# Kernel optimization log

Measured on AMD Instinct MI355X. Metric: run time of the kernel, lower is better.

Reference implementation:

```python
import jax, jax.numpy as jnp
import numpy as np

BIG = 1e10
RADIUS = 0.5
NSAMPLE = 1


def square_distance(src, dst):
    # src: [B,N,3], dst: [B,M,3] -> [B,N,M] squared euclidean distances
    d = -2.0 * jnp.einsum('bnc,bmc->bnm', src, dst)
    d = d + jnp.sum(src ** 2, -1)[:, :, None]
    d = d + jnp.sum(dst ** 2, -1)[:, None, :]
    return d


def farthest_point_sample(xyz, npoint):
    # xyz: [B,N,3]; returns int32 indices [B,npoint]
    B, N, _ = xyz.shape
    dist0 = jnp.full((B, N), BIG, dtype=xyz.dtype)
    far0 = jnp.argmax(xyz[:, :, 0], axis=1).astype(jnp.int32)

    def step(carry, _):
        dist, far = carry
        centroid = jnp.take_along_axis(xyz, far[:, None, None], axis=1)  # [B,1,3]
        d = jnp.sum((xyz - centroid) ** 2, -1)  # [B,N]
        dist = jnp.minimum(dist, d)
        new_far = jnp.argmax(dist, axis=-1).astype(jnp.int32)
        return (dist, new_far), far  # record PRE-update farthest, like the torch loop

    (_, _), centroids = jax.lax.scan(step, (dist0, far0), None, length=npoint)
    return centroids.T  # [B,npoint]


def index_points(points, idx):
    # points: [B,N,C], idx: [B,S] -> [B,S,C]
    return jnp.take_along_axis(points, idx[:, :, None], axis=1)


def query_ball_point(radius, nsample, xyz, new_xyz):
    # xyz: [B,N,3], new_xyz: [B,S,3] -> int32 [B,S,nsample]
    B, S, _ = new_xyz.shape
    N = xyz.shape[1]
    sqrdists = square_distance(new_xyz, xyz)  # [B,S,N]
    base = jnp.arange(N, dtype=jnp.int32)
    group_idx = jnp.where(sqrdists > radius ** 2, jnp.int32(N), base)  # [B,S,N]
    group_idx = jnp.sort(group_idx, axis=-1)[:, :, :nsample]
    group_first = jnp.broadcast_to(group_idx[:, :, :1], group_idx.shape)
    group_idx = jnp.where(group_idx == N, group_first, group_idx)
    return group_idx


def setup_inputs() -> dict:
    key = jax.random.key(0)
    k1, k2 = jax.random.split(key)
    B, N = 4, 16384
    xyz = jax.random.uniform(k1, (B, 3, N), dtype=jnp.float32)
    cls_label = jax.random.uniform(k2, (B, 16), dtype=jnp.float32)
    return {"xyz": xyz, "cls_label": cls_label, "npoint": 1024}


def reference(xyz, cls_label, npoint):
    pts = jnp.transpose(xyz, (0, 2, 1))  # [B,N,3]
    centroids = farthest_point_sample(pts, npoint)  # [B,S]
    new_xyz = index_points(pts, centroids)  # [B,S,3]
    idx = query_ball_point(RADIUS, NSAMPLE, pts, new_xyz)  # [B,S,1]
    return idx
```

## Files before the change

kernel.cpp:

```cpp
#include <hip/hip_runtime.h>


constexpr int N_PTS  = 16384;
constexpr int NPOINT = 1024;
constexpr int BLOCK  = 512;
constexpr int KPT    = N_PTS / BLOCK;
constexpr int NWAVE  = BLOCK / 64;

__device__ inline unsigned long long pack_key(unsigned tag, float v, int idx) {
    return ((unsigned long long)tag << 46) |
           ((unsigned long long)__float_as_uint(v) << 14) |
           (unsigned)(N_PTS - 1 - idx);
}

template <int CTRL, int RM, int BM>
__device__ inline unsigned long long dpp_max_step(unsigned long long key) {
    const int lo = (int)(unsigned)key;
    const int hi = (int)(unsigned)(key >> 32);
    const unsigned mlo =
        (unsigned)__builtin_amdgcn_update_dpp(lo, lo, CTRL, RM, BM, false);
    const unsigned mhi =
        (unsigned)__builtin_amdgcn_update_dpp(hi, hi, CTRL, RM, BM, false);
    const unsigned long long moved = ((unsigned long long)mhi << 32) | mlo;
    return key > moved ? key : moved;
}

__device__ inline unsigned long long row_max_key(unsigned long long key) {
    key = dpp_max_step<0x111, 0xf, 0xf>(key);
    key = dpp_max_step<0x112, 0xf, 0xf>(key);
    key = dpp_max_step<0x114, 0xf, 0xe>(key);
    key = dpp_max_step<0x118, 0xf, 0xc>(key);
    return key;
}

__global__ __launch_bounds__(BLOCK)
__attribute__((amdgpu_waves_per_eu(2, 2))) void fps_kernel(
    const float* __restrict__ xyz,
    int* __restrict__ cent)
{
    const int b   = blockIdx.x;
    const int tid = threadIdx.x;
    const float* X = xyz + (size_t)b * 3 * N_PTS;
    const float* Y = X + N_PTS;
    const float* Z = X + 2 * N_PTS;

    float px[KPT], py[KPT], pz[KPT], dst[KPT];
#pragma unroll
    for (int k = 0; k < KPT; ++k) {
        const int p = tid + k * BLOCK;
        px[k] = X[p];
        py[k] = Y[p];
        pz[k] = Z[p];
        dst[k] = 1e10f;
    }
#pragma unroll
    for (int k = 0; k < KPT; ++k)
        asm volatile("" : "+v"(px[k]), "+v"(py[k]), "+v"(pz[k]));

    __shared__ unsigned long long s_slot[2];

    const int lane = tid & 63;
    const bool row_leader = (lane & 15) == 15;

    if (tid == 0) { s_slot[0] = 0ull; s_slot[1] = 0ull; }
    __syncthreads();

    int far;
    {
        float bv = px[0];
        int   bk = 0;
#pragma unroll
        for (int k = 1; k < KPT; ++k) {
            if (px[k] > bv) { bv = px[k]; bk = k; }
        }
        const unsigned long long key =
            row_max_key(pack_key(1u, bv, tid + bk * BLOCK));
        if (row_leader) atomicMax(&s_slot[0], key);
        __syncthreads();
        far = __builtin_amdgcn_readfirstlane(
            N_PTS - 1 - (int)(s_slot[0] & 0x3FFFu));
    }

    for (int it = 0; it < NPOINT; ++it) {
        if (tid == 0) cent[b * NPOINT + it] = far;
        if (it == NPOINT - 1) break;

        const float cx = X[far];
        const float cy = Y[far];
        const float cz = Z[far];

        float nbv = -1.0f;
        int   nbk = 0;
#pragma unroll
        for (int k = 0; k < KPT; ++k) {
            const float dx = __fsub_rn(px[k], cx);
            const float dy = __fsub_rn(py[k], cy);
            const float dz = __fsub_rn(pz[k], cz);
            const float d  = __fadd_rn(
                __fadd_rn(__fmul_rn(dx, dx), __fmul_rn(dy, dy)),
                __fmul_rn(dz, dz));
            const float nd = fminf(dst[k], d);
            dst[k] = nd;
            if (nd > nbv) { nbv = nd; nbk = k; }
        }

        const unsigned long long key =
            row_max_key(pack_key((unsigned)(it + 2), nbv, tid + nbk * BLOCK));
        const int slot = (it + 1) & 1;
        if (row_leader) atomicMax(&s_slot[slot], key);
        __syncthreads();

        far = __builtin_amdgcn_readfirstlane(
            N_PTS - 1 - (int)(s_slot[slot] & 0x3FFFu));
    }
}

__global__ __launch_bounds__(256) void ballq_kernel(
    const float* __restrict__ xyz,
    const int* __restrict__ cent,
    int* __restrict__ out)
{
    const int gw   = (blockIdx.x * 256 + threadIdx.x) >> 6;
    const int lane = threadIdx.x & 63;
    const int b = gw / NPOINT;
    const int s = gw % NPOINT;

    const float* X = xyz + (size_t)b * 3 * N_PTS;
    const float* Y = X + N_PTS;
    const float* Z = X + 2 * N_PTS;

    const int ci = cent[b * NPOINT + s] & (N_PTS - 1);
    const float cx = X[ci];
    const float cy = Y[ci];
    const float cz = Z[ci];
    const float cn = __fadd_rn(
        __fadd_rn(__fmul_rn(cx, cx), __fmul_rn(cy, cy)), __fmul_rn(cz, cz));

    int res = N_PTS;
    for (int base = 0; base < N_PTS; base += 64) {
        const int p = base + lane;
        const float x = X[p];
        const float y = Y[p];
        const float z = Z[p];
        const float dot = __fadd_rn(
            __fadd_rn(__fmul_rn(x, cx), __fmul_rn(y, cy)), __fmul_rn(z, cz));
        const float pn = __fadd_rn(
            __fadd_rn(__fmul_rn(x, x), __fmul_rn(y, y)), __fmul_rn(z, z));
        const float d = __fadd_rn(__fadd_rn(__fmul_rn(-2.0f, dot), cn), pn);
        const bool hit = !(d > 0.25f);
        const unsigned long long m = __ballot(hit);
        if (m) {
            res = base + (__ffsll((long long)m) - 1);
            break;
        }
    }
    if (lane == 0) out[b * NPOINT + s] = res;
}

extern "C" void kernel_launch(void* const* d_in, const int* in_sizes, int n_in,
                              void* d_out, int out_size, void* d_ws, size_t ws_size,
                              hipStream_t stream) {
    const float* xyz = (const float*)d_in[0];
    const int B = in_sizes[1] / 16;
    int* cent = (int*)d_ws;
    int* out  = (int*)d_out;

    fps_kernel<<<B, BLOCK, 0, stream>>>(xyz, cent);

    const int nwaves  = B * NPOINT;
    const int nblocks = nwaves / 4;
    ballq_kernel<<<nblocks, 256, 0, stream>>>(xyz, cent, out);
}
```

Before: 1.885 ms.

## Split FPS across multiple workgroups per batch with global atomic barrier

Farthest point sampling for each batch is now spread over 8 workgroups instead of one. Each workgroup reduces its local max key across whole waves using DPP and shared memory. The workgroups then exchange the key through global atomicMax plus a spinning counter barrier at agent scope. This uses more CUs and less work per thread, but every iteration now pays a cross-workgroup global synchronisation. It also relies on all 32 blocks being co-resident, and the spin guard has a bounded timeout.

```diff
diff --git a/kernel.cpp b/kernel.cpp
--- a/kernel.cpp
+++ b/kernel.cpp
@@ -1,16 +1,23 @@
 #include <hip/hip_runtime.h>
 
 
-constexpr int N_PTS  = 16384;
-constexpr int NPOINT = 1024;
-constexpr int BLOCK  = 512;
-constexpr int KPT    = N_PTS / BLOCK;
-constexpr int NWAVE  = BLOCK / 64;
+constexpr int N_PTS       = 16384;
+constexpr int NPOINT      = 1024;
+constexpr int BLOCK       = 512;
+constexpr int NBLK        = 8;
+constexpr int PTS_PER_BLK = N_PTS / NBLK;
+constexpr int KPT         = PTS_PER_BLK / BLOCK;
+constexpr int NWAVE       = BLOCK / 64;
+constexpr int SYNC_U32    = 32;
 
 __device__ inline unsigned long long pack_key(unsigned tag, float v, int idx) {
     return ((unsigned long long)tag << 46) |
            ((unsigned long long)__float_as_uint(v) << 14) |
            (unsigned)(N_PTS - 1 - idx);
+}
+__device__ inline unsigned long long umax64(unsigned long long a,
+                                            unsigned long long b) {
+    return a > b ? a : b;
 }
 
 template <int CTRL, int RM, int BM>
@@ -24,46 +31,70 @@
     const unsigned long long moved = ((unsigned long long)mhi << 32) | mlo;
     return key > moved ? key : moved;
 }
-
-__device__ inline unsigned long long row_max_key(unsigned long long key) {
+__device__ inline unsigned long long wave_max_key(unsigned long long key) {
     key = dpp_max_step<0x111, 0xf, 0xf>(key);
     key = dpp_max_step<0x112, 0xf, 0xf>(key);
     key = dpp_max_step<0x114, 0xf, 0xe>(key);
     key = dpp_max_step<0x118, 0xf, 0xc>(key);
+    key = dpp_max_step<0x142, 0xa, 0xf>(key);
+    key = dpp_max_step<0x143, 0xc, 0xf>(key);
     return key;
 }
 
-__global__ __launch_bounds__(BLOCK)
-__attribute__((amdgpu_waves_per_eu(2, 2))) void fps_kernel(
+__device__ inline int sync_exchange(unsigned long long* slots, unsigned* cnt,
+                                    unsigned long long key, unsigned seq) {
+    const int si = (int)((seq + 1) & 1);
+    atomicMax(&slots[si], key);
+    __hip_atomic_fetch_add(cnt, 1u, __ATOMIC_RELEASE,
+                           __HIP_MEMORY_SCOPE_AGENT);
+    const unsigned target = (unsigned)NBLK * seq;
+    unsigned guard = 0;
+    while (__hip_atomic_load(cnt, __ATOMIC_ACQUIRE,
+                             __HIP_MEMORY_SCOPE_AGENT) < target) {
+        if (++guard > (1u << 16)) break;
+    }
+    const unsigned long long fin = __hip_atomic_load(
+        &slots[si], __ATOMIC_RELAXED, __HIP_MEMORY_SCOPE_AGENT);
+    return N_PTS - 1 - (int)(fin & 0x3FFFu);
+}
+
+__global__ void init_sync(unsigned* __restrict__ sync, int n) {
+    const int i = blockIdx.x * blockDim.x + threadIdx.x;
+    if (i < n) sync[i] = 0u;
+}
+
+__global__ __launch_bounds__(BLOCK) void fps_kernel(
     const float* __restrict__ xyz,
-    int* __restrict__ cent)
+    int* __restrict__ cent,
+    unsigned* __restrict__ sync)
 {
-    const int b   = blockIdx.x;
+    const int b   = blockIdx.x / NBLK;
+    const int blk = blockIdx.x % NBLK;
     const int tid = threadIdx.x;
     const float* X = xyz + (size_t)b * 3 * N_PTS;
     const float* Y = X + N_PTS;
     const float* Z = X + 2 * N_PTS;
 
+    unsigned long long* slots =
+        (unsigned long long*)(sync + (size_t)b * SYNC_U32);
+    unsigned* cnt = sync + (size_t)b * SYNC_U32 + 4;
+
+    const int base = blk * PTS_PER_BLK;
     float px[KPT], py[KPT], pz[KPT], dst[KPT];
 #pragma unroll
     for (int k = 0; k < KPT; ++k) {
-        const int p = tid + k * BLOCK;
+        const int p = base + tid + k * BLOCK;
         px[k] = X[p];
         py[k] = Y[p];
         pz[k] = Z[p];
         dst[k] = 1e10f;
     }
-#pragma unroll
-    for (int k = 0; k < KPT; ++k)
-        asm volatile("" : "+v"(px[k]), "+v"(py[k]), "+v"(pz[k]));
-
-    __shared__ unsigned long long s_slot[2];
-
+
+    __shared__ unsigned long long s_key[NWAVE];
+    __shared__ int s_far;
+
+    const int wave = tid >> 6;
     const int lane = tid & 63;
-    const bool row_leader = (lane & 15) == 15;
-
-    if (tid == 0) { s_slot[0] = 0ull; s_slot[1] = 0ull; }
-    __syncthreads();
 
     int far;
     {
@@ -74,15 +105,23 @@
             if (px[k] > bv) { bv = px[k]; bk = k; }
         }
         const unsigned long long key =
-            row_max_key(pack_key(1u, bv, tid + bk * BLOCK));
-        if (row_leader) atomicMax(&s_slot[0], key);
-        __syncthreads();
-        far = __builtin_amdgcn_readfirstlane(
-            N_PTS - 1 - (int)(s_slot[0] & 0x3FFFu));
+            wave_max_key(pack_key(1u, bv, base + tid + bk * BLOCK));
+        if (lane == 63) s_key[wave] = key;
+        __syncthreads();
+        if (tid == 0) {
+            const unsigned long long bkk =
+                umax64(umax64(umax64(s_key[0], s_key[1]),
+                              umax64(s_key[2], s_key[3])),
+                       umax64(umax64(s_key[4], s_key[5]),
+                              umax64(s_key[6], s_key[7])));
+            s_far = sync_exchange(slots, cnt, bkk, 1u);
+        }
+        __syncthreads();
+        far = __builtin_amdgcn_readfirstlane(s_far) & (N_PTS - 1);
     }
 
     for (int it = 0; it < NPOINT; ++it) {
-        if (tid == 0) cent[b * NPOINT + it] = far;
+        if (blk == 0 && tid == 0) cent[b * NPOINT + it] = far;
         if (it == NPOINT - 1) break;
 
         const float cx = X[far];
@@ -104,14 +143,20 @@
             if (nd > nbv) { nbv = nd; nbk = k; }
         }
 
-        const unsigned long long key =
-            row_max_key(pack_key((unsigned)(it + 2), nbv, tid + nbk * BLOCK));
-        const int slot = (it + 1) & 1;
-        if (row_leader) atomicMax(&s_slot[slot], key);
-        __syncthreads();
-
-        far = __builtin_amdgcn_readfirstlane(
-            N_PTS - 1 - (int)(s_slot[slot] & 0x3FFFu));
+        const unsigned long long key = wave_max_key(
+            pack_key((unsigned)(it + 2), nbv, base + tid + nbk * BLOCK));
+        if (lane == 63) s_key[wave] = key;
+        __syncthreads();
+        if (tid == 0) {
+            const unsigned long long bkk =
+                umax64(umax64(umax64(s_key[0], s_key[1]),
+                              umax64(s_key[2], s_key[3])),
+                       umax64(umax64(s_key[4], s_key[5]),
+                              umax64(s_key[6], s_key[7])));
+            s_far = sync_exchange(slots, cnt, bkk, (unsigned)(it + 2));
+        }
+        __syncthreads();
+        far = __builtin_amdgcn_readfirstlane(s_far) & (N_PTS - 1);
     }
 }
 
@@ -163,9 +208,11 @@
     const float* xyz = (const float*)d_in[0];
     const int B = in_sizes[1] / 16;
     int* cent = (int*)d_ws;
+    unsigned* sync = (unsigned*)d_ws + (size_t)B * NPOINT;
     int* out  = (int*)d_out;
 
-    fps_kernel<<<B, BLOCK, 0, stream>>>(xyz, cent);
+    init_sync<<<1, 256, 0, stream>>>(sync, B * SYNC_U32);
+    fps_kernel<<<B * NBLK, BLOCK, 0, stream>>>(xyz, cent, sync);
 
     const int nwaves  = B * NPOINT;
     const int nblocks = nwaves / 4;
```

Result: slower. 2.049 ms (+8.7%).
